# Kernel tuning notes

Measured on AMD Instinct MI355X. Metric: run time of the kernel, lower is better.

## Reference

```python
import jax, jax.numpy as jnp
import numpy as np
import math

BATCH, SEQLEN, DMODEL, NSTATE, DFF = 4, 2048, 1024, 16, 4096
EPS = 1e-6


def rmsnorm(x, scale):
    return x * jax.lax.rsqrt(jnp.mean(x * x, axis=-1, keepdims=True) + EPS) * scale


def ssm_scan(u, A_ssm, B_ssm, C_ssm, D_ssm):
    # u: (B, L, D). Diagonal SSM per (d, n) channel/state pair.
    dt = jnp.exp(jnp.linspace(math.log(0.001), math.log(0.1), NSTATE))  # (N,)
    expA = jnp.exp(A_ssm)                 # (D, N); continuous A = -expA
    dA = jnp.exp(-expA * dt)              # (D, N) discrete decay
    dB = B_ssm * (1.0 - dA) / expA        # (D, N) ZOH input matrix

    def step(s, u_t):
        # s: (B, D, N), u_t: (B, D)
        s = s * dA + u_t[..., None] * dB
        y = jnp.einsum('bdn,dn->bd', s, C_ssm)
        return s, y

    s0 = jnp.zeros((u.shape[0], DMODEL, NSTATE), dtype=u.dtype)
    _, ys = jax.lax.scan(step, s0, jnp.transpose(u, (1, 0, 2)))  # ys: (L, B, D)
    return jnp.transpose(ys, (1, 0, 2)) + u * D_ssm


def setup_inputs() -> dict:
    key = jax.random.key(0)
    ks = jax.random.split(key, 6)
    return {
        'x': jax.random.normal(ks[0], (BATCH, SEQLEN, DMODEL), jnp.float32),
        'A_ssm': jax.random.normal(ks[1], (DMODEL, NSTATE), jnp.float32),
        'B_ssm': jax.random.normal(ks[2], (DMODEL, NSTATE), jnp.float32),
        'C_ssm': jax.random.normal(ks[3], (DMODEL, NSTATE), jnp.float32),
        'D_ssm': jnp.zeros((DMODEL,), jnp.float32),
        'scale1': jnp.ones((DMODEL,), jnp.float32),
        'scale2': jnp.ones((DMODEL,), jnp.float32),
        'w1': jax.random.normal(ks[4], (DMODEL, DFF), jnp.float32) * 0.02,
        'b1': jnp.zeros((DFF,), jnp.float32),
        'w2': jax.random.normal(ks[5], (DFF, DMODEL), jnp.float32) * 0.02,
        'b2': jnp.zeros((DMODEL,), jnp.float32),
    }


def reference(x, A_ssm, B_ssm, C_ssm, D_ssm, scale1, scale2, w1, b1, w2, b2):
    x = x + ssm_scan(rmsnorm(x, scale1), A_ssm, B_ssm, C_ssm, D_ssm)
    h = rmsnorm(x, scale2)
    h = jax.nn.gelu(h @ w1 + b1, approximate=False) @ w2 + b2
    return x + h
```

## Files before the change

### kernel.cpp

```cpp
#include <hip/hip_runtime.h>
#include <cstdint>
#include <cstddef>


#define BATCH 4
#define SEQLEN 2048
#define DMODEL 1024
#define NSTATE 16
#define DFF 4096
#define NCH 32
#define LCH 64

typedef unsigned short ushort_t;
typedef __attribute__((ext_vector_type(8))) short short8;
typedef __attribute__((ext_vector_type(4))) float f32x4;

__device__ __forceinline__ ushort_t f2bf(float f) {
  uint32_t u = __builtin_bit_cast(uint32_t, f);
  uint32_t r = (u + 0x7FFFu + ((u >> 16) & 1u)) >> 16;
  return (ushort_t)r;
}

__global__ void coef_kernel(const float* __restrict__ A_ssm, const float* __restrict__ B_ssm,
                            const float* __restrict__ C_ssm,
                            float* __restrict__ dA_t, float* __restrict__ dBz_t,
                            float* __restrict__ dAc_t, float* __restrict__ Ct) {
  int d = blockIdx.x * 256 + threadIdx.x;
  if (d >= DMODEL) return;
  const float l0 = -6.907755278982137f;
  const float ld = 0.30701134573253947f;
  for (int n = 0; n < NSTATE; n++) {
    float dt = expf(l0 + (float)n * ld);
    float a  = A_ssm[d * NSTATE + n];
    float ea = expf(a);
    float da = expf(-ea * dt);
    float dbz = B_ssm[d * NSTATE + n] * (1.f - da) / ea;
    float dac = expf(-ea * dt * (float)LCH);
    dA_t [n * DMODEL + d] = da;
    dBz_t[n * DMODEL + d] = dbz;
    dAc_t[n * DMODEL + d] = dac;
    Ct   [n * DMODEL + d] = C_ssm[d * NSTATE + n];
  }
}

__global__ void transpose_to_bf16(const float* __restrict__ src, ushort_t* __restrict__ dst,
                                  int R, int C) {
  __shared__ float tile[32][33];
  int bx = blockIdx.x * 32, by = blockIdx.y * 32;
  int tx = threadIdx.x, ty = threadIdx.y;
  #pragma unroll
  for (int i = 0; i < 4; i++) {
    int r = by + ty + i * 8;
    tile[ty + i * 8][tx] = src[(size_t)r * C + bx + tx];
  }
  __syncthreads();
  #pragma unroll
  for (int i = 0; i < 4; i++) {
    int c = bx + ty + i * 8;
    dst[(size_t)c * R + by + tx] = f2bf(tile[tx][ty + i * 8]);
  }
}

__global__ void rms1_kernel(const float* __restrict__ x, float* __restrict__ rrms) {
  int row = blockIdx.x * 4 + (threadIdx.x >> 6);
  int lane = threadIdx.x & 63;
  const float4* p = (const float4*)(x + (size_t)row * DMODEL);
  float s = 0.f;
  #pragma unroll
  for (int w = 0; w < 4; w++) {
    float4 v = p[w * 64 + lane];
    s += v.x * v.x + v.y * v.y + v.z * v.z + v.w * v.w;
  }
  #pragma unroll
  for (int off = 32; off; off >>= 1) s += __shfl_xor(s, off, 64);
  if (lane == 0) rrms[row] = rsqrtf(s * (1.f / DMODEL) + 1e-6f);
}

__global__ void scan_pass1(const float* __restrict__ x, const float* __restrict__ rrms,
                           const float* __restrict__ scale1,
                           const float* __restrict__ dA_t, const float* __restrict__ dBz_t,
                           float* __restrict__ s_fin) {
  int d = blockIdx.x * 256 + threadIdx.x;
  int b = blockIdx.y, c = blockIdx.z;
  float dA[NSTATE], dBz[NSTATE], s[NSTATE];
  #pragma unroll
  for (int n = 0; n < NSTATE; n++) {
    dA[n] = dA_t[n * DMODEL + d];
    dBz[n] = dBz_t[n * DMODEL + d];
    s[n] = 0.f;
  }
  float sc1 = scale1[d];
  const float* xp = x + ((size_t)b * SEQLEN + (size_t)c * LCH) * DMODEL + d;
  const float* rp = rrms + b * SEQLEN + c * LCH;
  for (int t = 0; t < LCH; t++) {
    float u = xp[(size_t)t * DMODEL] * rp[t] * sc1;
    #pragma unroll
    for (int n = 0; n < NSTATE; n++) s[n] = fmaf(s[n], dA[n], u * dBz[n]);
  }
  #pragma unroll
  for (int n = 0; n < NSTATE; n++)
    s_fin[(((size_t)n * BATCH + b) * NCH + c) * DMODEL + d] = s[n];
}

__global__ void scan_pass2(const float* __restrict__ s_fin, const float* __restrict__ dAc_t,
                           float* __restrict__ s_in) {
  int idx = blockIdx.x * 256 + threadIdx.x;
  int d = idx & (DMODEL - 1);
  int b = (idx >> 10) & (BATCH - 1);
  int n = idx >> 12;
  float dc = dAc_t[n * DMODEL + d];
  float s = 0.f;
  for (int c = 0; c < NCH; c++) {
    size_t o = (((size_t)n * BATCH + b) * NCH + c) * DMODEL + d;
    s_in[o] = s;
    s = s_fin[o] + dc * s;
  }
}

__global__ void scan_pass3(const float* __restrict__ x, const float* __restrict__ rrms,
                           const float* __restrict__ scale1,
                           const float* __restrict__ dA_t, const float* __restrict__ dBz_t,
                           const float* __restrict__ Ct, const float* __restrict__ Dv,
                           const float* __restrict__ s_in, float* __restrict__ out) {
  int d = blockIdx.x * 256 + threadIdx.x;
  int b = blockIdx.y, c = blockIdx.z;
  float dA[NSTATE], dBz[NSTATE], Cc[NSTATE], s[NSTATE];
  #pragma unroll
  for (int n = 0; n < NSTATE; n++) {
    dA[n] = dA_t[n * DMODEL + d];
    dBz[n] = dBz_t[n * DMODEL + d];
    Cc[n] = Ct[n * DMODEL + d];
    s[n] = s_in[(((size_t)n * BATCH + b) * NCH + c) * DMODEL + d];
  }
  float sc1 = scale1[d], Dd = Dv[d];
  const float* xp = x + ((size_t)b * SEQLEN + (size_t)c * LCH) * DMODEL + d;
  const float* rp = rrms + b * SEQLEN + c * LCH;
  float* op = out + ((size_t)b * SEQLEN + (size_t)c * LCH) * DMODEL + d;
  for (int t = 0; t < LCH; t++) {
    float xv = xp[(size_t)t * DMODEL];
    float u = xv * rp[t] * sc1;
    float y = 0.f;
    #pragma unroll
    for (int n = 0; n < NSTATE; n++) {
      s[n] = fmaf(s[n], dA[n], u * dBz[n]);
      y = fmaf(Cc[n], s[n], y);
    }
    op[(size_t)t * DMODEL] = xv + y + u * Dd;
  }
}

__global__ void rms2_kernel(const float* __restrict__ x2, const float* __restrict__ scale2,
                            ushort_t* __restrict__ hb) {
  int row = blockIdx.x * 4 + (threadIdx.x >> 6);
  int lane = threadIdx.x & 63;
  const float4* p = (const float4*)(x2 + (size_t)row * DMODEL);
  float4 v[4];
  float s = 0.f;
  #pragma unroll
  for (int w = 0; w < 4; w++) {
    v[w] = p[w * 64 + lane];
    s += v[w].x * v[w].x + v[w].y * v[w].y + v[w].z * v[w].z + v[w].w * v[w].w;
  }
  #pragma unroll
  for (int off = 32; off; off >>= 1) s += __shfl_xor(s, off, 64);
  float r = rsqrtf(s * (1.f / DMODEL) + 1e-6f);
  const float4* sc = (const float4*)scale2;
  #pragma unroll
  for (int w = 0; w < 4; w++) {
    float4 scv = sc[w * 64 + lane];
    ushort4 u;
    u.x = f2bf(v[w].x * r * scv.x);
    u.y = f2bf(v[w].y * r * scv.y);
    u.z = f2bf(v[w].z * r * scv.z);
    u.w = f2bf(v[w].w * r * scv.w);
    *(ushort4*)(hb + (size_t)row * DMODEL + (size_t)(w * 64 + lane) * 4) = u;
  }
}


#define BKG 32

template <int N>
__device__ __forceinline__ void fence_vm() {
  asm volatile("s_waitcnt vmcnt(%0)" :: "n"(N) : "memory");
}

__device__ __forceinline__ void bar() { asm volatile("s_barrier" ::: "memory"); }

__device__ __forceinline__ void gl2lds16(const ushort_t* g, ushort_t* l) {
  __builtin_amdgcn_global_load_lds(
      (const __attribute__((address_space(1))) unsigned int*)g,
      (__attribute__((address_space(3))) unsigned int*)l, 16, 0, 0);
}

template <int BM, int BN, int WM, int WN, int MODE, int K>
__global__ __launch_bounds__(512, 2) void gemm_cv(const ushort_t* __restrict__ A,
                                                  const ushort_t* __restrict__ B,
                                                  const float* __restrict__ bias,
                                                  const float* __restrict__ resid,
                                                  void* __restrict__ outp,
                                                  int M, int N) {
  constexpr int NSLOT = 4;
  constexpr int TILEA = BM * BKG;
  constexpr int TILEB = BN * BKG;
  constexpr int SLOT  = TILEA + TILEB;
  constexpr int NA = BM / 128;
  constexpr int NB = BN / 128;
  constexpr int LPT = NA + NB;
  constexpr int MR = BM / (WM * 16);
  constexpr int NR = BN / (WN * 16);
  constexpr int NT = K / BKG;
  __shared__ __align__(16) ushort_t lds[NSLOT * SLOT];

  const int tid = threadIdx.x;
  const int wave = tid >> 6, lane = tid & 63;
  const int wr = wave / WN, wc = wave % WN;

  const int nwg = gridDim.x;
  const int cpx = nwg >> 3;
  const int bid = blockIdx.x;
  const int wg  = (bid & 7) * cpx + (bid >> 3);
  const int nbn = N / BN;
  const int m0 = (wg / nbn) * BM;
  const int n0 = (wg % nbn) * BN;

  const int scol = 8 * ((tid & 3) ^ ((tid >> 3) & 3));
  const ushort_t* aB = A + (size_t)(m0 + (tid >> 2)) * K + scol;
  const ushort_t* bB = B + (size_t)(n0 + (tid >> 2)) * K + scol;
  const int waveOff = wave * 512;

  auto stage = [&](int slot, int t) {
    ushort_t* sA = lds + slot * SLOT;
    ushort_t* sB = sA + TILEA;
    #pragma unroll
    for (int j = 0; j < NA; j++)
      gl2lds16(aB + (size_t)t * BKG + (size_t)j * 128 * K, sA + j * 4096 + waveOff);
    #pragma unroll
    for (int j = 0; j < NB; j++)
      gl2lds16(bB + (size_t)t * BKG + (size_t)j * 128 * K, sB + j * 4096 + waveOff);
  };

  f32x4 acc[MR][NR] = {};

  stage(0, 0); stage(1, 1); stage(2, 2);
  fence_vm<2 * LPT>();
  bar();

  const int r = lane & 15;
  const int cswz = ((lane >> 4) * 8) ^ (((r >> 1) & 3) << 3);

  #pragma unroll 2
  for (int t = 0; t < NT; ++t) {
    const ushort_t* sA = lds + (t & 3) * SLOT;
    const ushort_t* sB = sA + TILEA;

    short8 bfr[NR], af[MR];
    #pragma unroll
    for (int n = 0; n < NR; n++)
      bfr[n] = *(const short8*)(sB + (size_t)(wc * (BN / WN) + n * 16 + r) * BKG + cswz);
    #pragma unroll
    for (int m = 0; m < MR; m++)
      af[m] = *(const short8*)(sA + (size_t)(wr * (BM / WM) + m * 16 + r) * BKG + cswz);

    if (t + 3 < NT) stage((t + 3) & 3, t + 3);

    if (t + 3 < NT)      fence_vm<2 * LPT>();
    else if (t + 2 < NT) fence_vm<LPT>();
    else if (t + 1 < NT) fence_vm<0>();
    bar();

    __builtin_amdgcn_s_setprio(1);
    #pragma unroll
    for (int m = 0; m < MR; m++)
      #pragma unroll
      for (int n = 0; n < NR; n++)
        acc[m][n] = __builtin_amdgcn_mfma_f32_16x16x32_bf16(af[m], bfr[n], acc[m][n], 0, 0, 0);
    __builtin_amdgcn_s_setprio(0);
    bar();
  }

  const int colb = n0 + wc * (BN / WN) + r;
  const int rowb = m0 + wr * (BM / WM) + ((lane >> 4) << 2);
  #pragma unroll
  for (int n = 0; n < NR; n++) {
    int col = colb + n * 16;
    float bs = bias[col];
    #pragma unroll
    for (int m = 0; m < MR; m++) {
      int row = rowb + m * 16;
      #pragma unroll
      for (int j = 0; j < 4; j++) {
        float v = acc[m][n][j] + bs;
        size_t o = (size_t)(row + j) * N + col;
        if (MODE == 1) {
          float g = 0.5f * v * (1.f + erff(v * 0.70710678118654752f));
          ((ushort_t*)outp)[o] = f2bf(g);
        } else {
          ((float*)outp)[o] = resid[o] + v;
        }
      }
    }
  }
}

extern "C" void kernel_launch(void* const* d_in, const int* in_sizes, int n_in,
                              void* d_out, int out_size, void* d_ws, size_t ws_size,
                              hipStream_t stream) {
  (void)in_sizes; (void)n_in; (void)out_size; (void)ws_size;
  const float* x      = (const float*)d_in[0];
  const float* A_ssm  = (const float*)d_in[1];
  const float* B_ssm  = (const float*)d_in[2];
  const float* C_ssm  = (const float*)d_in[3];
  const float* D_ssm  = (const float*)d_in[4];
  const float* scale1 = (const float*)d_in[5];
  const float* scale2 = (const float*)d_in[6];
  const float* w1     = (const float*)d_in[7];
  const float* b1     = (const float*)d_in[8];
  const float* w2     = (const float*)d_in[9];
  const float* b2     = (const float*)d_in[10];
  float* out = (float*)d_out;

  char* ws = (char*)d_ws;
  float*    rrms  = (float*)(ws + 0);
  float*    dA_t  = (float*)(ws + 32768);
  float*    dBz_t = (float*)(ws + 98304);
  float*    dAc_t = (float*)(ws + 163840);
  float*    Ct    = (float*)(ws + 229376);
  float*    s_fin = (float*)(ws + 294912);
  float*    s_in  = (float*)(ws + 8683520);
  ushort_t* hb    = (ushort_t*)(ws + 17072128);
  ushort_t* w1t   = (ushort_t*)(ws + 33849344);
  ushort_t* w2t   = (ushort_t*)(ws + 42237952);
  ushort_t* gb    = (ushort_t*)(ws + 50626560);

  const int ROWS = BATCH * SEQLEN;

  coef_kernel<<<DMODEL / 256, 256, 0, stream>>>(A_ssm, B_ssm, C_ssm, dA_t, dBz_t, dAc_t, Ct);
  transpose_to_bf16<<<dim3(DFF / 32, DMODEL / 32), dim3(32, 8), 0, stream>>>(w1, w1t, DMODEL, DFF);
  transpose_to_bf16<<<dim3(DMODEL / 32, DFF / 32), dim3(32, 8), 0, stream>>>(w2, w2t, DFF, DMODEL);
  rms1_kernel<<<ROWS / 4, 256, 0, stream>>>(x, rrms);
  scan_pass1<<<dim3(DMODEL / 256, BATCH, NCH), 256, 0, stream>>>(x, rrms, scale1, dA_t, dBz_t, s_fin);
  scan_pass2<<<(BATCH * DMODEL * NSTATE) / 256, 256, 0, stream>>>(s_fin, dAc_t, s_in);
  scan_pass3<<<dim3(DMODEL / 256, BATCH, NCH), 256, 0, stream>>>(x, rrms, scale1, dA_t, dBz_t, Ct,
                                                                 D_ssm, s_in, out);
  rms2_kernel<<<ROWS / 4, 256, 0, stream>>>(out, scale2, hb);

  gemm_cv<256, 256, 2, 4, 1, DMODEL><<<(ROWS / 256) * (DFF / 256), 512, 0, stream>>>(
      hb, w1t, b1, nullptr, gb, ROWS, DFF);
  gemm_cv<256, 128, 4, 2, 2, DFF><<<(ROWS / 256) * (DMODEL / 128), 512, 0, stream>>>(
      gb, w2t, b2, out, out, ROWS, DMODEL);
}
```

Baseline: 240.8 us.

## Shrink GEMM tiles to 128x128 with 256 threads and 3-stage pipeline

Replaces the templated 256x256/256x128 GEMM tiling (512 threads, 4-slot LDS ring, prefetch depth 3) with a fixed 128x128 tile on 256 threads (4 waves, 64x64 per wave), a 3-slot LDS ring and prefetch depth 2. The wait and barrier now sit after the MFMA block, so there is one barrier per iteration instead of two. The aim is more workgroups for better CU fill and cheaper synchronisation. In exchange, arithmetic intensity per tile drops and global/L2 traffic rises, and the shallower prefetch leaves less latency hidden.

```diff
diff --git a/kernel.cpp b/kernel.cpp
--- a/kernel.cpp
+++ b/kernel.cpp
@@ -193,28 +193,23 @@
       (__attribute__((address_space(3))) unsigned int*)l, 16, 0, 0);
 }
 
-template <int BM, int BN, int WM, int WN, int MODE, int K>
-__global__ __launch_bounds__(512, 2) void gemm_cv(const ushort_t* __restrict__ A,
-                                                  const ushort_t* __restrict__ B,
-                                                  const float* __restrict__ bias,
-                                                  const float* __restrict__ resid,
-                                                  void* __restrict__ outp,
-                                                  int M, int N) {
-  constexpr int NSLOT = 4;
+template <int MODE, int K>
+__global__ __launch_bounds__(256) void gemm_cv(const ushort_t* __restrict__ A,
+                                               const ushort_t* __restrict__ B,
+                                               const float* __restrict__ bias,
+                                               const float* __restrict__ resid,
+                                               void* __restrict__ outp,
+                                               int M, int N) {
+  constexpr int BM = 128, BN = 128;
   constexpr int TILEA = BM * BKG;
-  constexpr int TILEB = BN * BKG;
-  constexpr int SLOT  = TILEA + TILEB;
-  constexpr int NA = BM / 128;
-  constexpr int NB = BN / 128;
-  constexpr int LPT = NA + NB;
-  constexpr int MR = BM / (WM * 16);
-  constexpr int NR = BN / (WN * 16);
-  constexpr int NT = K / BKG;
-  __shared__ __align__(16) ushort_t lds[NSLOT * SLOT];
+  constexpr int SLOT  = TILEA * 2;
+  constexpr int LPT   = 4;
+  constexpr int NT    = K / BKG;
+  __shared__ __align__(16) ushort_t lds[3 * SLOT];
 
   const int tid = threadIdx.x;
   const int wave = tid >> 6, lane = tid & 63;
-  const int wr = wave / WN, wc = wave % WN;
+  const int wr = wave >> 1, wc = wave & 1;
 
   const int nwg = gridDim.x;
   const int cpx = nwg >> 3;
@@ -233,60 +228,63 @@
     ushort_t* sA = lds + slot * SLOT;
     ushort_t* sB = sA + TILEA;
     #pragma unroll
-    for (int j = 0; j < NA; j++)
-      gl2lds16(aB + (size_t)t * BKG + (size_t)j * 128 * K, sA + j * 4096 + waveOff);
-    #pragma unroll
-    for (int j = 0; j < NB; j++)
-      gl2lds16(bB + (size_t)t * BKG + (size_t)j * 128 * K, sB + j * 4096 + waveOff);
+    for (int j = 0; j < 2; j++)
+      gl2lds16(aB + (size_t)t * BKG + (size_t)j * 64 * K, sA + j * 2048 + waveOff);
+    #pragma unroll
+    for (int j = 0; j < 2; j++)
+      gl2lds16(bB + (size_t)t * BKG + (size_t)j * 64 * K, sB + j * 2048 + waveOff);
   };
 
-  f32x4 acc[MR][NR] = {};
-
-  stage(0, 0); stage(1, 1); stage(2, 2);
-  fence_vm<2 * LPT>();
+  f32x4 acc[4][4] = {};
+
+  stage(0, 0); stage(1, 1);
+  fence_vm<LPT>();
   bar();
 
   const int r = lane & 15;
   const int cswz = ((lane >> 4) * 8) ^ (((r >> 1) & 3) << 3);
 
-  #pragma unroll 2
+  int s0 = 0;
   for (int t = 0; t < NT; ++t) {
-    const ushort_t* sA = lds + (t & 3) * SLOT;
+    const ushort_t* sA = lds + s0 * SLOT;
     const ushort_t* sB = sA + TILEA;
 
-    short8 bfr[NR], af[MR];
-    #pragma unroll
-    for (int n = 0; n < NR; n++)
-      bfr[n] = *(const short8*)(sB + (size_t)(wc * (BN / WN) + n * 16 + r) * BKG + cswz);
-    #pragma unroll
-    for (int m = 0; m < MR; m++)
-      af[m] = *(const short8*)(sA + (size_t)(wr * (BM / WM) + m * 16 + r) * BKG + cswz);
-
-    if (t + 3 < NT) stage((t + 3) & 3, t + 3);
-
-    if (t + 3 < NT)      fence_vm<2 * LPT>();
-    else if (t + 2 < NT) fence_vm<LPT>();
-    else if (t + 1 < NT) fence_vm<0>();
-    bar();
+    short8 bfr[4], af[4];
+    #pragma unroll
+    for (int n = 0; n < 4; n++)
+      bfr[n] = *(const short8*)(sB + (size_t)(wc * 64 + n * 16 + r) * BKG + cswz);
+    #pragma unroll
+    for (int m = 0; m < 4; m++)
+      af[m] = *(const short8*)(sA + (size_t)(wr * 64 + m * 16 + r) * BKG + cswz);
+
+    if (t + 2 < NT) {
+      int s2 = s0 + 2; if (s2 >= 3) s2 -= 3;
+      stage(s2, t + 2);
+    }
 
     __builtin_amdgcn_s_setprio(1);
     #pragma unroll
-    for (int m = 0; m < MR; m++)
+    for (int m = 0; m < 4; m++)
       #pragma unroll
-      for (int n = 0; n < NR; n++)
+      for (int n = 0; n < 4; n++)
         acc[m][n] = __builtin_amdgcn_mfma_f32_16x16x32_bf16(af[m], bfr[n], acc[m][n], 0, 0, 0);
     __builtin_amdgcn_s_setprio(0);
+
+    if (t + 2 < NT) fence_vm<LPT>();
+    else            fence_vm<0>();
     bar();
-  }
-
-  const int colb = n0 + wc * (BN / WN) + r;
-  const int rowb = m0 + wr * (BM / WM) + ((lane >> 4) << 2);
-  #pragma unroll
-  for (int n = 0; n < NR; n++) {
+
+    s0 = (s0 == 2) ? 0 : s0 + 1;
+  }
+
+  const int colb = n0 + wc * 64 + r;
+  const int rowb = m0 + wr * 64 + ((lane >> 4) << 2);
+  #pragma unroll
+  for (int n = 0; n < 4; n++) {
     int col = colb + n * 16;
     float bs = bias[col];
     #pragma unroll
-    for (int m = 0; m < MR; m++) {
+    for (int m = 0; m < 4; m++) {
       int row = rowb + m * 16;
       #pragma unroll
       for (int j = 0; j < 4; j++) {
@@ -345,8 +343,8 @@
                                                                  D_ssm, s_in, out);
   rms2_kernel<<<ROWS / 4, 256, 0, stream>>>(out, scale2, hb);
 
-  gemm_cv<256, 256, 2, 4, 1, DMODEL><<<(ROWS / 256) * (DFF / 256), 512, 0, stream>>>(
+  gemm_cv<1, DMODEL><<<(ROWS / 128) * (DFF / 128), 256, 0, stream>>>(
       hb, w1t, b1, nullptr, gb, ROWS, DFF);
-  gemm_cv<256, 128, 4, 2, 2, DFF><<<(ROWS / 256) * (DMODEL / 128), 512, 0, stream>>>(
+  gemm_cv<2, DFF><<<(ROWS / 128) * (DMODEL / 128), 256, 0, stream>>>(
       gb, w2t, b2, out, out, ROWS, DMODEL);
 }
```

Result: slower. 255.1 us (+6.0%).
